# Kernel optimization log

Measured on AMD Instinct MI355X. Metric: run time of the kernel, lower is better.

## Reference

```python
import jax, jax.numpy as jnp
import numpy as np

EPS = 1e-5

def _layer_norm(x, g, b):
    mu = jnp.mean(x, axis=-1, keepdims=True)
    var = jnp.mean(jnp.square(x - mu), axis=-1, keepdims=True)
    return (x - mu) * jax.lax.rsqrt(var + EPS) * g + b

def setup_inputs() -> dict:
    key = jax.random.key(0)
    ks = jax.random.split(key, 8)
    B, S, H, NH, FF = 2, 2048, 2048, 16, 8192
    x = jax.random.normal(ks[0], (B, S, H), dtype=jnp.float32)
    # causal mask: True = masked (matches masked_fill semantics)
    mask = jnp.triu(jnp.ones((S, S), dtype=bool), k=1)
    sc = 0.02
    wq = jax.random.normal(ks[1], (H, H), dtype=jnp.float32) * sc
    wk = jax.random.normal(ks[2], (H, H), dtype=jnp.float32) * sc
    wv = jax.random.normal(ks[3], (H, H), dtype=jnp.float32) * sc
    wo = jax.random.normal(ks[4], (H, H), dtype=jnp.float32) * sc
    w_in = jax.random.normal(ks[5], (H, FF), dtype=jnp.float32) * sc
    w_out = jax.random.normal(ks[6], (FF, H), dtype=jnp.float32) * sc
    ln1_g = jnp.ones((H,), jnp.float32); ln1_b = jnp.zeros((H,), jnp.float32)
    ln2_g = jnp.ones((H,), jnp.float32); ln2_b = jnp.zeros((H,), jnp.float32)
    return {"x": x, "mask": mask, "wq": wq, "wk": wk, "wv": wv, "wo": wo,
            "w_in": w_in, "w_out": w_out,
            "ln1_g": ln1_g, "ln1_b": ln1_b, "ln2_g": ln2_g, "ln2_b": ln2_b}

def reference(x, mask, wq, wk, wv, wo, w_in, w_out, ln1_g, ln1_b, ln2_g, ln2_b):
    B, S, H = x.shape
    NH = 16
    HD = H // NH
    scale = HD ** (-0.5)
    # attention with pre-norm
    xn = _layer_norm(x, ln1_g, ln1_b)
    q = (xn @ wq).reshape(B, S, NH, HD)
    k = (xn @ wk).reshape(B, S, NH, HD)
    v = (xn @ wv).reshape(B, S, NH, HD)
    scores = jnp.einsum('bqhd,bkhd->bhqk', q, k) * scale
    scores = jnp.where(mask[:S, :S], -jnp.inf, scores)
    attn = jax.nn.softmax(scores, axis=-1)
    out = jnp.einsum('bhqk,bkhd->bqhd', attn, v).reshape(B, S, H)
    h = x + out @ wo
    # FFN with pre-norm, tanh-approx GELU
    hn = _layer_norm(h, ln2_g, ln2_b)
    ff = jax.nn.gelu(hn @ w_in, approximate=True) @ w_out
    return h + ff
```

## Files before the change

kernel.cpp:

```cpp
#include <hip/hip_runtime.h>
#include <hip/hip_bf16.h>

#define B_ 2
#define S_ 2048
#define H_ 2048
#define NH_ 16
#define HD_ 128
#define FF_ 8192

typedef __attribute__((ext_vector_type(8))) short bf16x8;
typedef __attribute__((ext_vector_type(4))) float f32x4;

#define NEG_BIG (-1e30f)

#define GLL16(gp, lp)                                                                    \
  __builtin_amdgcn_global_load_lds((const __attribute__((address_space(1))) void*)(gp),  \
                                   (__attribute__((address_space(3))) void*)(lp), 16, 0, 0)

__device__ __forceinline__ float b2f(unsigned short u) {
  union { unsigned int i; float f; } c; c.i = ((unsigned int)u) << 16; return c.f;
}
__device__ __forceinline__ unsigned short f2b(float f) {
  unsigned int u = __float_as_uint(f);
  u += 0x7fffu + ((u >> 16) & 1u);
  return (unsigned short)(u >> 16);
}
__device__ __forceinline__ float ldf(const void* p, size_t i, int f32) {
  return f32 ? ((const float*)p)[i] : b2f(((const unsigned short*)p)[i]);
}
__device__ __forceinline__ void unpack8(uint4 r, float* f) {
  f[0] = b2f((unsigned short)(r.x & 0xffffu)); f[1] = b2f((unsigned short)(r.x >> 16));
  f[2] = b2f((unsigned short)(r.y & 0xffffu)); f[3] = b2f((unsigned short)(r.y >> 16));
  f[4] = b2f((unsigned short)(r.z & 0xffffu)); f[5] = b2f((unsigned short)(r.z >> 16));
  f[6] = b2f((unsigned short)(r.w & 0xffffu)); f[7] = b2f((unsigned short)(r.w >> 16));
}

__global__ void detect_k(const unsigned int* __restrict__ x, int* __restrict__ flagp) {
  if (threadIdx.x == 0) {
    int c = 0;
    for (int i = 0; i < 256; ++i) {
      unsigned int e = (x[i] >> 7) & 0xffu;
      c += (e >= 97u && e <= 130u) ? 1 : 0;
    }
    *flagp = (c < 128) ? 1 : 0;
  }
}

__global__ __launch_bounds__(256) void transpose_k(const void* __restrict__ in,
                                                   unsigned short* __restrict__ out,
                                                   int R, int C,
                                                   const int* __restrict__ flagp) {
  __shared__ unsigned short tile[32][33];
  int f32 = *flagp;
  int r0 = blockIdx.y * 32, c0 = blockIdx.x * 32;
  int tx = threadIdx.x & 31, ty = threadIdx.x >> 5;
#pragma unroll
  for (int p = 0; p < 4; ++p)
    tile[ty + p * 8][tx] = f2b(ldf(in, (size_t)(r0 + ty + p * 8) * C + c0 + tx, f32));
  __syncthreads();
#pragma unroll
  for (int p = 0; p < 4; ++p)
    out[(size_t)(c0 + ty + p * 8) * R + r0 + tx] = tile[tx][ty + p * 8];
}

__global__ __launch_bounds__(256) void v_transpose_k(const unsigned short* __restrict__ qkv,
                                                     unsigned short* __restrict__ VT) {
  __shared__ unsigned short tile[32][33];
  int bh = blockIdx.z;
  int b = bh >> 4, h = bh & 15;
  int s0 = blockIdx.x * 32, d0 = blockIdx.y * 32;
  int tx = threadIdx.x & 31, ty = threadIdx.x >> 5;
#pragma unroll
  for (int p = 0; p < 4; ++p) {
    int s = s0 + ty + p * 8;
    tile[ty + p * 8][tx] = qkv[(size_t)(b * S_ + s) * (3 * H_) + 2 * H_ + h * HD_ + d0 + tx];
  }
  __syncthreads();
#pragma unroll
  for (int p = 0; p < 4; ++p)
    VT[((size_t)bh * HD_ + d0 + ty + p * 8) * S_ + s0 + tx] = tile[tx][ty + p * 8];
}

__global__ __launch_bounds__(256) void ln_k(const void* __restrict__ x,
                                            const void* __restrict__ g,
                                            const void* __restrict__ b,
                                            unsigned short* __restrict__ y,
                                            const int* __restrict__ flagp, int in_mode) {
  __shared__ float red[2][4];
  int f32 = *flagp;
  int xf = in_mode ? f32 : 0;
  int row = blockIdx.x;
  int t = threadIdx.x;
  float v[8];
  size_t base = (size_t)row * H_ + t * 8;
  if (xf) {
    const float4* p = reinterpret_cast<const float4*>((const float*)x + base);
    float4 u0 = p[0], u1 = p[1];
    v[0] = u0.x; v[1] = u0.y; v[2] = u0.z; v[3] = u0.w;
    v[4] = u1.x; v[5] = u1.y; v[6] = u1.z; v[7] = u1.w;
  } else {
    unpack8(*reinterpret_cast<const uint4*>((const unsigned short*)x + base), v);
  }
  float s1 = 0.f, s2 = 0.f;
#pragma unroll
  for (int i = 0; i < 8; ++i) { s1 += v[i]; s2 += v[i] * v[i]; }
#pragma unroll
  for (int off = 32; off > 0; off >>= 1) {
    s1 += __shfl_down(s1, off);
    s2 += __shfl_down(s2, off);
  }
  int w = t >> 6, lane = t & 63;
  if (lane == 0) { red[0][w] = s1; red[1][w] = s2; }
  __syncthreads();
  s1 = red[0][0] + red[0][1] + red[0][2] + red[0][3];
  s2 = red[1][0] + red[1][1] + red[1][2] + red[1][3];
  float mu = s1 * (1.0f / H_);
  float var = s2 * (1.0f / H_) - mu * mu;
  float rinv = rsqrtf(var + 1e-5f);
  float gv[8], bv[8];
#pragma unroll
  for (int i = 0; i < 8; ++i) {
    gv[i] = ldf(g, t * 8 + i, f32);
    bv[i] = ldf(b, t * 8 + i, f32);
  }
  unsigned int o[4];
#pragma unroll
  for (int i = 0; i < 4; ++i) {
    unsigned short lo = f2b((v[2 * i] - mu) * rinv * gv[2 * i] + bv[2 * i]);
    unsigned short hi = f2b((v[2 * i + 1] - mu) * rinv * gv[2 * i + 1] + bv[2 * i + 1]);
    o[i] = (unsigned int)lo | ((unsigned int)hi << 16);
  }
  uint4 ov; ov.x = o[0]; ov.y = o[1]; ov.z = o[2]; ov.w = o[3];
  *reinterpret_cast<uint4*>(y + base) = ov;
}

template <int EPI>
__global__ __launch_bounds__(256) void gemm_bt(const unsigned short* __restrict__ A,
                                               const unsigned short* __restrict__ BT,
                                               void* __restrict__ C,
                                               const void* __restrict__ resid,
                                               int M, int N, int K,
                                               const int* __restrict__ flagp,
                                               int resid_mode, int store_mode) {
  __shared__ unsigned short As[2][128 * 32];
  __shared__ unsigned short Bs[2][128 * 32];
  int f32 = *flagp;
  int rf = resid_mode ? f32 : 0;
  int sf = store_mode ? f32 : 0;
  int tid = threadIdx.x;
  int m_base = blockIdx.y * 128;
  int n_base = blockIdx.x * 128;
  int w = tid >> 6, lane = tid & 63;
  int l15 = lane & 15, quad = lane >> 4;
  int wm = (w >> 1) * 64, wn = (w & 1) * 64;
  int lr = lane >> 2, lc = lane & 3;
  int swz = lc ^ (lr & 3);

  const unsigned short* gA0 = A + (size_t)(m_base + w * 32 + lr) * K + swz * 8;
  const unsigned short* gA1 = A + (size_t)(m_base + w * 32 + 16 + lr) * K + swz * 8;
  const unsigned short* gB0 = BT + (size_t)(n_base + w * 32 + lr) * K + swz * 8;
  const unsigned short* gB1 = BT + (size_t)(n_base + w * 32 + 16 + lr) * K + swz * 8;
  int lofs0 = (w * 32) * 32;
  int lofs1 = (w * 32 + 16) * 32;

  f32x4 acc[4][4];
#pragma unroll
  for (int i = 0; i < 4; ++i)
#pragma unroll
    for (int j = 0; j < 4; ++j) acc[i][j] = (f32x4){0.f, 0.f, 0.f, 0.f};

  int rd_swz = (quad ^ (l15 & 3)) * 8;

  GLL16(gA0, &As[0][lofs0]);
  GLL16(gA1, &As[0][lofs1]);
  GLL16(gB0, &Bs[0][lofs0]);
  GLL16(gB1, &Bs[0][lofs1]);

  int cur = 0;
  for (int k0 = 0; k0 < K; k0 += 32, cur ^= 1) {
    __syncthreads();
    int k1 = k0 + 32;
    if (k1 < K) {
      GLL16(gA0 + k1, &As[cur ^ 1][lofs0]);
      GLL16(gA1 + k1, &As[cur ^ 1][lofs1]);
      GLL16(gB0 + k1, &Bs[cur ^ 1][lofs0]);
      GLL16(gB1 + k1, &Bs[cur ^ 1][lofs1]);
    }
    bf16x8 a[4], b[4];
#pragma unroll
    for (int i = 0; i < 4; ++i)
      a[i] = *reinterpret_cast<const bf16x8*>(&As[cur][(wm + i * 16 + l15) * 32 + rd_swz]);
#pragma unroll
    for (int j = 0; j < 4; ++j)
      b[j] = *reinterpret_cast<const bf16x8*>(&Bs[cur][(wn + j * 16 + l15) * 32 + rd_swz]);
#pragma unroll
    for (int i = 0; i < 4; ++i)
#pragma unroll
      for (int j = 0; j < 4; ++j)
        acc[i][j] = __builtin_amdgcn_mfma_f32_16x16x32_bf16(a[i], b[j], acc[i][j], 0, 0, 0);
  }

#pragma unroll
  for (int i = 0; i < 4; ++i) {
#pragma unroll
    for (int j = 0; j < 4; ++j) {
#pragma unroll
      for (int r = 0; r < 4; ++r) {
        int row = m_base + wm + i * 16 + quad * 4 + r;
        int col = n_base + wn + j * 16 + l15;
        size_t idx = (size_t)row * N + col;
        float v = acc[i][j][r];
        if (EPI == 1) v += ldf(resid, idx, rf);
        if (EPI == 2) {
          float u = v;
          float tt = 0.7978845608028654f * (u + 0.044715f * u * u * u);
          v = 0.5f * u * (1.0f + tanhf(tt));
        }
        if (sf) ((float*)C)[idx] = v;
        else    ((unsigned short*)C)[idx] = f2b(v);
      }
    }
  }
}

__global__ __launch_bounds__(256) void attn_k(const unsigned short* __restrict__ qkv,
                                              const unsigned short* __restrict__ VT,
                                              unsigned short* __restrict__ out) {
  __shared__ unsigned short Ks[64 * 128];
  __shared__ unsigned short Vs[128 * 64];
  __shared__ unsigned short Ps[4][16][72];
  int qb = blockIdx.x, bh = blockIdx.y;
  int b = bh >> 4, h = bh & 15;
  int q0 = qb * 64;
  int tid = threadIdx.x;
  int w = tid >> 6, lane = tid & 63, l15 = lane & 15, quad = lane >> 4;
  const float scale = 0.08838834764831845f;

  bf16x8 aq[4];
  {
    const unsigned short* qrow =
        qkv + (size_t)(b * S_ + q0 + w * 16 + l15) * (3 * H_) + h * HD_;
#pragma unroll
    for (int ks = 0; ks < 4; ++ks)
      aq[ks] = *reinterpret_cast<const bf16x8*>(qrow + ks * 32 + quad * 8);
  }

  int krow_off = lane >> 4;
  int kcb = lane & 15;
  int vrow_off = lane >> 3;
  int vcb = lane & 7;

  f32x4 o[8];
#pragma unroll
  for (int f = 0; f < 8; ++f) o[f] = (f32x4){0.f, 0.f, 0.f, 0.f};
  float m_i[4], l_i[4];
#pragma unroll
  for (int r = 0; r < 4; ++r) { m_i[r] = NEG_BIG; l_i[r] = 0.f; }

  const unsigned short* kbase = qkv + (size_t)b * S_ * (3 * H_) + H_ + h * HD_;
  const unsigned short* vbase = VT + (size_t)bh * HD_ * S_;

  for (int kv0 = 0; kv0 <= q0; kv0 += 64) {
    __syncthreads();
#pragma unroll
    for (int t = 0; t < 4; ++t) {
      int krow = w * 16 + t * 4 + krow_off;
      int kswz = kcb ^ (krow & 7);
      GLL16(kbase + (size_t)(kv0 + krow) * (3 * H_) + kswz * 8, &Ks[(w * 16 + t * 4) * 128]);
      int vrow = w * 32 + t * 8 + vrow_off;
      int vswz = vcb ^ (vrow & 7);
      GLL16(vbase + (size_t)vrow * S_ + kv0 + vswz * 8, &Vs[(w * 32 + t * 8) * 64]);
    }
    __syncthreads();

    f32x4 sc[4];
#pragma unroll
    for (int j = 0; j < 4; ++j) sc[j] = (f32x4){0.f, 0.f, 0.f, 0.f};
#pragma unroll
    for (int ks = 0; ks < 4; ++ks) {
#pragma unroll
      for (int j = 0; j < 4; ++j) {
        int r = j * 16 + l15;
        bf16x8 bk = *reinterpret_cast<const bf16x8*>(
            &Ks[r * 128 + (((ks * 4 + quad) ^ (l15 & 7))) * 8]);
        sc[j] = __builtin_amdgcn_mfma_f32_16x16x32_bf16(aq[ks], bk, sc[j], 0, 0, 0);
      }
    }
    bool diag = (kv0 == q0);
#pragma unroll
    for (int j = 0; j < 4; ++j)
#pragma unroll
      for (int r = 0; r < 4; ++r) {
        float s = sc[j][r] * scale;
        if (diag && (j * 16 + l15 > w * 16 + quad * 4 + r)) s = NEG_BIG;
        sc[j][r] = s;
      }

    float mx[4];
#pragma unroll
    for (int r = 0; r < 4; ++r) {
      mx[r] = sc[0][r];
#pragma unroll
      for (int j = 1; j < 4; ++j) mx[r] = fmaxf(mx[r], sc[j][r]);
    }
#pragma unroll
    for (int mm = 1; mm <= 8; mm <<= 1)
#pragma unroll
      for (int r = 0; r < 4; ++r) mx[r] = fmaxf(mx[r], __shfl_xor(mx[r], mm));
    float alpha[4];
#pragma unroll
    for (int r = 0; r < 4; ++r) {
      float mn = fmaxf(m_i[r], mx[r]);
      alpha[r] = __expf(m_i[r] - mn);
      m_i[r] = mn;
    }
    float pr[4][4], rs[4] = {0.f, 0.f, 0.f, 0.f};
#pragma unroll
    for (int j = 0; j < 4; ++j)
#pragma unroll
      for (int r = 0; r < 4; ++r) {
        float p = __expf(sc[j][r] - m_i[r]);
        pr[j][r] = p;
        rs[r] += p;
      }
#pragma unroll
    for (int mm = 1; mm <= 8; mm <<= 1)
#pragma unroll
      for (int r = 0; r < 4; ++r) rs[r] += __shfl_xor(rs[r], mm);
#pragma unroll
    for (int r = 0; r < 4; ++r) l_i[r] = l_i[r] * alpha[r] + rs[r];
#pragma unroll
    for (int f = 0; f < 8; ++f)
#pragma unroll
      for (int r = 0; r < 4; ++r) o[f][r] *= alpha[r];

#pragma unroll
    for (int j = 0; j < 4; ++j)
#pragma unroll
      for (int r = 0; r < 4; ++r)
        Ps[w][quad * 4 + r][j * 16 + l15] = f2b(pr[j][r]);

#pragma unroll
    for (int ks2 = 0; ks2 < 2; ++ks2) {
      bf16x8 ap = *reinterpret_cast<const bf16x8*>(&Ps[w][l15][ks2 * 32 + quad * 8]);
#pragma unroll
      for (int f = 0; f < 8; ++f) {
        int r = f * 16 + l15;
        bf16x8 bv = *reinterpret_cast<const bf16x8*>(
            &Vs[r * 64 + (((ks2 * 4 + quad) ^ (l15 & 7))) * 8]);
        o[f] = __builtin_amdgcn_mfma_f32_16x16x32_bf16(ap, bv, o[f], 0, 0, 0);
      }
    }
  }

  float inv[4];
#pragma unroll
  for (int r = 0; r < 4; ++r) inv[r] = 1.0f / l_i[r];
#pragma unroll
  for (int f = 0; f < 8; ++f)
#pragma unroll
    for (int r = 0; r < 4; ++r)
      out[(size_t)(b * S_ + q0 + w * 16 + quad * 4 + r) * H_ + h * HD_ + f * 16 + l15] =
          f2b(o[f][r] * inv[r]);
}

extern "C" void kernel_launch(void* const* d_in, const int* in_sizes, int n_in,
                              void* d_out, int out_size, void* d_ws, size_t ws_size,
                              hipStream_t stream) {
  (void)in_sizes; (void)n_in; (void)out_size; (void)ws_size;
  const void* x     = d_in[0];
  const void* wq    = d_in[2];
  const void* wk    = d_in[3];
  const void* wv    = d_in[4];
  const void* wo    = d_in[5];
  const void* w_in  = d_in[6];
  const void* w_out = d_in[7];
  const void* g1    = d_in[8];
  const void* b1    = d_in[9];
  const void* g2    = d_in[10];
  const void* b2    = d_in[11];
  char* ws = (char*)d_ws;

  const size_t MB = 1024 * 1024;
  unsigned short* W  = (unsigned short*)(ws + 0 * MB);
  unsigned short* E  = (unsigned short*)(ws + 32 * MB);
  unsigned short* F  = (unsigned short*)(ws + 48 * MB);
  unsigned short* Hb = (unsigned short*)(ws + 112 * MB);
  int* flagp         = (int*)(ws + 128 * MB);

  unsigned short* wqkvT = W;
  unsigned short* xn    = E;
  unsigned short* qkv   = F;
  unsigned short* VT    = F + (size_t)B_ * S_ * 3 * H_;
  unsigned short* attnb = E;
  unsigned short* hbuf  = Hb;
  unsigned short* hn    = E;
  unsigned short* ff1   = F;

  dim3 blk(256);
  detect_k<<<1, 64, 0, stream>>>((const unsigned int*)x, flagp);
  transpose_k<<<dim3(H_ / 32, H_ / 32), blk, 0, stream>>>(wq, wqkvT, H_, H_, flagp);
  transpose_k<<<dim3(H_ / 32, H_ / 32), blk, 0, stream>>>(wk, wqkvT + (size_t)H_ * H_, H_, H_, flagp);
  transpose_k<<<dim3(H_ / 32, H_ / 32), blk, 0, stream>>>(wv, wqkvT + (size_t)2 * H_ * H_, H_, H_, flagp);
  ln_k<<<B_ * S_, blk, 0, stream>>>(x, g1, b1, xn, flagp, 1);
  gemm_bt<0><<<dim3(3 * H_ / 128, B_ * S_ / 128), blk, 0, stream>>>(
      xn, wqkvT, qkv, nullptr, B_ * S_, 3 * H_, H_, flagp, 0, 0);
  v_transpose_k<<<dim3(S_ / 32, HD_ / 32, B_ * NH_), blk, 0, stream>>>(qkv, VT);
  attn_k<<<dim3(S_ / 64, B_ * NH_), blk, 0, stream>>>(qkv, VT, attnb);
  transpose_k<<<dim3(H_ / 32, H_ / 32), blk, 0, stream>>>(wo, W, H_, H_, flagp);
  gemm_bt<1><<<dim3(H_ / 128, B_ * S_ / 128), blk, 0, stream>>>(
      attnb, W, hbuf, x, B_ * S_, H_, H_, flagp, 1, 0);
  ln_k<<<B_ * S_, blk, 0, stream>>>(hbuf, g2, b2, hn, flagp, 0);
  transpose_k<<<dim3(FF_ / 32, H_ / 32), blk, 0, stream>>>(w_in, W, H_, FF_, flagp);
  gemm_bt<2><<<dim3(FF_ / 128, B_ * S_ / 128), blk, 0, stream>>>(
      hn, W, ff1, nullptr, B_ * S_, FF_, H_, flagp, 0, 0);
  transpose_k<<<dim3(H_ / 32, FF_ / 32), blk, 0, stream>>>(w_out, W, FF_, H_, flagp);
  gemm_bt<1><<<dim3(H_ / 128, B_ * S_ / 128), blk, 0, stream>>>(
      ff1, W, d_out, hbuf, B_ * S_, H_, FF_, flagp, 0, 1);
}
```

Before: 1.088 ms.

## Replace GEMM with 256x256-tile, 8-wave ping-pong pipelined kernel and XCD-aware block remap

```diff
diff --git a/kernel.cpp b/kernel.cpp
--- a/kernel.cpp
+++ b/kernel.cpp
@@ -134,82 +134,148 @@
   *reinterpret_cast<uint4*>(y + base) = ov;
 }
 
+#define PH_BAR() do { asm volatile("" ::: "memory"); __builtin_amdgcn_s_barrier(); \
+                      asm volatile("" ::: "memory"); } while (0)
+#define VMC(n) asm volatile("s_waitcnt vmcnt(" #n ")" ::: "memory")
+
+#define STA(buf_, h_, kt_) do {                                                        \
+  GLL16(pA0 + (size_t)(h_) * 128 * K + (kt_) * 64, &LdsA[buf_][(h_) * 8192 + lw]);     \
+  GLL16(pA1 + (size_t)(h_) * 128 * K + (kt_) * 64, &LdsA[buf_][(h_) * 8192 + 4096 + lw]); } while (0)
+#define STB(buf_, h_, kt_) do {                                                        \
+  GLL16(pB0 + (size_t)(h_) * 128 * K + (kt_) * 64, &LdsB[buf_][(h_) * 8192 + lw]);     \
+  GLL16(pB1 + (size_t)(h_) * 128 * K + (kt_) * 64, &LdsB[buf_][(h_) * 8192 + 4096 + lw]); } while (0)
+
+#define LDA4(AF, buf_, mb_) do { _Pragma("unroll")                                     \
+  for (int mi_ = 0; mi_ < 4; ++mi_) {                                                  \
+    const unsigned short* _p = &LdsA[buf_][(wr * 128 + ((mb_) + mi_) * 16 + l15) * 64];\
+    AF[mi_][0] = *reinterpret_cast<const bf16x8*>(_p + cs0);                           \
+    AF[mi_][1] = *reinterpret_cast<const bf16x8*>(_p + cs1); } } while (0)
+#define LDB2(BF, buf_, nb_) do { _Pragma("unroll")                                     \
+  for (int ni_ = 0; ni_ < 2; ++ni_) {                                                  \
+    const unsigned short* _p = &LdsB[buf_][(wc * 64 + ((nb_) + ni_) * 16 + l15) * 64]; \
+    BF[ni_][0] = *reinterpret_cast<const bf16x8*>(_p + cs0);                           \
+    BF[ni_][1] = *reinterpret_cast<const bf16x8*>(_p + cs1); } } while (0)
+
+#define MF8(AF, BF, MO, NO) do { _Pragma("unroll")                                     \
+  for (int mi_ = 0; mi_ < 4; ++mi_) { _Pragma("unroll")                                \
+    for (int ni_ = 0; ni_ < 2; ++ni_) {                                                \
+      acc[(MO) + mi_][(NO) + ni_] = __builtin_amdgcn_mfma_f32_16x16x32_bf16(           \
+          AF[mi_][0], BF[ni_][0], acc[(MO) + mi_][(NO) + ni_], 0, 0, 0);               \
+      acc[(MO) + mi_][(NO) + ni_] = __builtin_amdgcn_mfma_f32_16x16x32_bf16(           \
+          AF[mi_][1], BF[ni_][1], acc[(MO) + mi_][(NO) + ni_], 0, 0, 0);               \
+    } } } while (0)
+
+#define GITER(LAST, tO, tE2, tO2) do {                                                 \
+                                                                              \
+  LDA4(aL, 0, 0); LDB2(bL, 0, 0);                                                      \
+  STA(1, 1, tO);                                                                       \
+  PH_BAR(); __builtin_amdgcn_s_setprio(1);                                             \
+  MF8(aL, bL, 0, 0);                                                                   \
+  __builtin_amdgcn_s_setprio(0); PH_BAR();                                             \
+                                                                              \
+  LDB2(bH, 0, 2);                                                                      \
+  PH_BAR(); __builtin_amdgcn_s_setprio(1);                                             \
+  MF8(aL, bH, 0, 2);                                                                   \
+  __builtin_amdgcn_s_setprio(0); PH_BAR();                                             \
+                                                                              \
+  LDA4(aH, 0, 4);                                                                      \
+  if (!(LAST)) STB(0, 0, tE2);                                                         \
+  PH_BAR(); __builtin_amdgcn_s_setprio(1);                                             \
+  MF8(aH, bL, 4, 0);                                                                   \
+  __builtin_amdgcn_s_setprio(0); PH_BAR();                                             \
+                                                                              \
+  if (!(LAST)) { STB(0, 1, tE2); STA(0, 0, tE2); VMC(6); } else { VMC(0); }            \
+  PH_BAR(); __builtin_amdgcn_s_setprio(1);                                             \
+  MF8(aH, bH, 4, 2);                                                                   \
+  __builtin_amdgcn_s_setprio(0); PH_BAR();                                             \
+                                                                              \
+  LDA4(aL, 1, 0); LDB2(bL, 1, 0);                                                      \
+  if (!(LAST)) STA(0, 1, tE2);                                                         \
+  PH_BAR(); __builtin_amdgcn_s_setprio(1);                                             \
+  MF8(aL, bL, 0, 0);                                                                   \
+  __builtin_amdgcn_s_setprio(0); PH_BAR();                                             \
+                                                                              \
+  LDB2(bH, 1, 2);                                                                      \
+  PH_BAR(); __builtin_amdgcn_s_setprio(1);                                             \
+  MF8(aL, bH, 0, 2);                                                                   \
+  __builtin_amdgcn_s_setprio(0); PH_BAR();                                             \
+                                                                              \
+  LDA4(aH, 1, 4);                                                                      \
+  if (!(LAST)) STB(1, 0, tO2);                                                         \
+  PH_BAR(); __builtin_amdgcn_s_setprio(1);                                             \
+  MF8(aH, bL, 4, 0);                                                                   \
+  __builtin_amdgcn_s_setprio(0); PH_BAR();                                             \
+                                                                              \
+  if (!(LAST)) { STB(1, 1, tO2); STA(1, 0, tO2); VMC(6); }                             \
+  PH_BAR(); __builtin_amdgcn_s_setprio(1);                                             \
+  MF8(aH, bH, 4, 2);                                                                   \
+  __builtin_amdgcn_s_setprio(0); PH_BAR();                                             \
+} while (0)
+
 template <int EPI>
-__global__ __launch_bounds__(256) void gemm_bt(const unsigned short* __restrict__ A,
+__global__ __launch_bounds__(512) void gemm256(const unsigned short* __restrict__ A,
                                                const unsigned short* __restrict__ BT,
                                                void* __restrict__ C,
                                                const void* __restrict__ resid,
                                                int M, int N, int K,
                                                const int* __restrict__ flagp,
-                                               int resid_mode, int store_mode) {
-  __shared__ unsigned short As[2][128 * 32];
-  __shared__ unsigned short Bs[2][128 * 32];
+                                               int resid_mode, int store_mode, int nbx) {
+  (void)M;
+  __shared__ unsigned short LdsA[2][16384];
+  __shared__ unsigned short LdsB[2][16384];
+
+  unsigned nwg = gridDim.x, q = nwg >> 3;
+  unsigned o = blockIdx.x;
+  unsigned wg = (o & 7u) * q + (o >> 3);
+  int bx = (int)(wg % (unsigned)nbx), by = (int)(wg / (unsigned)nbx);
+  int m_base = by * 256, n_base = bx * 256;
+
+  int tid = threadIdx.x;
+  int w = tid >> 6, lane = tid & 63;
+  int l15 = lane & 15, quad = lane >> 4;
+  int wr = w >> 2, wc = w & 3;
+
+  int row0 = w * 8 + (lane >> 3);
+  int scb  = (lane & 7) ^ (lane >> 3);
+  const unsigned short* pA0 = A + (size_t)(m_base + row0) * K + scb * 8;
+  const unsigned short* pA1 = pA0 + (size_t)64 * K;
+  const unsigned short* pB0 = BT + (size_t)(n_base + row0) * K + scb * 8;
+  const unsigned short* pB1 = pB0 + (size_t)64 * K;
+  unsigned lw = (unsigned)w * 512;
+
+  int cs0 = ((quad) ^ (l15 & 7)) * 8;
+  int cs1 = ((4 + quad) ^ (l15 & 7)) * 8;
+
+  f32x4 acc[8][4];
+#pragma unroll
+  for (int i = 0; i < 8; ++i)
+#pragma unroll
+    for (int j = 0; j < 4; ++j) acc[i][j] = (f32x4){0.f, 0.f, 0.f, 0.f};
+
+  bf16x8 aL[4][2], aH[4][2], bL[2][2], bH[2][2];
+
+  STA(0, 0, 0); STA(0, 1, 0); STB(0, 0, 0); STB(0, 1, 0);
+  STB(1, 0, 1); STB(1, 1, 1); STA(1, 0, 1);
+  VMC(6);
+  PH_BAR();
+
+  int niter = K >> 7;
+  for (int i = 0; i < niter - 1; ++i) GITER(0, 2 * i + 1, 2 * i + 2, 2 * i + 3);
+  GITER(1, 2 * niter - 1, 0, 0);
+
   int f32 = *flagp;
   int rf = resid_mode ? f32 : 0;
   int sf = store_mode ? f32 : 0;
-  int tid = threadIdx.x;
-  int m_base = blockIdx.y * 128;
-  int n_base = blockIdx.x * 128;
-  int w = tid >> 6, lane = tid & 63;
-  int l15 = lane & 15, quad = lane >> 4;
-  int wm = (w >> 1) * 64, wn = (w & 1) * 64;
-  int lr = lane >> 2, lc = lane & 3;
-  int swz = lc ^ (lr & 3);
-
-  const unsigned short* gA0 = A + (size_t)(m_base + w * 32 + lr) * K + swz * 8;
-  const unsigned short* gA1 = A + (size_t)(m_base + w * 32 + 16 + lr) * K + swz * 8;
-  const unsigned short* gB0 = BT + (size_t)(n_base + w * 32 + lr) * K + swz * 8;
-  const unsigned short* gB1 = BT + (size_t)(n_base + w * 32 + 16 + lr) * K + swz * 8;
-  int lofs0 = (w * 32) * 32;
-  int lofs1 = (w * 32 + 16) * 32;
-
-  f32x4 acc[4][4];
-#pragma unroll
-  for (int i = 0; i < 4; ++i)
-#pragma unroll
-    for (int j = 0; j < 4; ++j) acc[i][j] = (f32x4){0.f, 0.f, 0.f, 0.f};
-
-  int rd_swz = (quad ^ (l15 & 3)) * 8;
-
-  GLL16(gA0, &As[0][lofs0]);
-  GLL16(gA1, &As[0][lofs1]);
-  GLL16(gB0, &Bs[0][lofs0]);
-  GLL16(gB1, &Bs[0][lofs1]);
-
-  int cur = 0;
-  for (int k0 = 0; k0 < K; k0 += 32, cur ^= 1) {
-    __syncthreads();
-    int k1 = k0 + 32;
-    if (k1 < K) {
-      GLL16(gA0 + k1, &As[cur ^ 1][lofs0]);
-      GLL16(gA1 + k1, &As[cur ^ 1][lofs1]);
-      GLL16(gB0 + k1, &Bs[cur ^ 1][lofs0]);
-      GLL16(gB1 + k1, &Bs[cur ^ 1][lofs1]);
-    }
-    bf16x8 a[4], b[4];
-#pragma unroll
-    for (int i = 0; i < 4; ++i)
-      a[i] = *reinterpret_cast<const bf16x8*>(&As[cur][(wm + i * 16 + l15) * 32 + rd_swz]);
-#pragma unroll
-    for (int j = 0; j < 4; ++j)
-      b[j] = *reinterpret_cast<const bf16x8*>(&Bs[cur][(wn + j * 16 + l15) * 32 + rd_swz]);
-#pragma unroll
-    for (int i = 0; i < 4; ++i)
-#pragma unroll
-      for (int j = 0; j < 4; ++j)
-        acc[i][j] = __builtin_amdgcn_mfma_f32_16x16x32_bf16(a[i], b[j], acc[i][j], 0, 0, 0);
-  }
-
-#pragma unroll
-  for (int i = 0; i < 4; ++i) {
-#pragma unroll
-    for (int j = 0; j < 4; ++j) {
+#pragma unroll
+  for (int mi = 0; mi < 8; ++mi) {
+#pragma unroll
+    for (int ni = 0; ni < 4; ++ni) {
 #pragma unroll
       for (int r = 0; r < 4; ++r) {
-        int row = m_base + wm + i * 16 + quad * 4 + r;
-        int col = n_base + wn + j * 16 + l15;
+        int row = m_base + wr * 128 + mi * 16 + quad * 4 + r;
+        int col = n_base + wc * 64 + ni * 16 + l15;
         size_t idx = (size_t)row * N + col;
-        float v = acc[i][j][r];
+        float v = acc[mi][ni][r];
         if (EPI == 1) v += ldf(resid, idx, rf);
         if (EPI == 2) {
           float u = v;
@@ -398,23 +464,24 @@
   unsigned short* ff1   = F;
 
   dim3 blk(256);
+  dim3 gblk(512);
   detect_k<<<1, 64, 0, stream>>>((const unsigned int*)x, flagp);
   transpose_k<<<dim3(H_ / 32, H_ / 32), blk, 0, stream>>>(wq, wqkvT, H_, H_, flagp);
   transpose_k<<<dim3(H_ / 32, H_ / 32), blk, 0, stream>>>(wk, wqkvT + (size_t)H_ * H_, H_, H_, flagp);
   transpose_k<<<dim3(H_ / 32, H_ / 32), blk, 0, stream>>>(wv, wqkvT + (size_t)2 * H_ * H_, H_, H_, flagp);
   ln_k<<<B_ * S_, blk, 0, stream>>>(x, g1, b1, xn, flagp, 1);
-  gemm_bt<0><<<dim3(3 * H_ / 128, B_ * S_ / 128), blk, 0, stream>>>(
-      xn, wqkvT, qkv, nullptr, B_ * S_, 3 * H_, H_, flagp, 0, 0);
+  gemm256<0><<<dim3((3 * H_ / 256) * (B_ * S_ / 256)), gblk, 0, stream>>>(
+      xn, wqkvT, qkv, nullptr, B_ * S_, 3 * H_, H_, flagp, 0, 0, 3 * H_ / 256);
   v_transpose_k<<<dim3(S_ / 32, HD_ / 32, B_ * NH_), blk, 0, stream>>>(qkv, VT);
   attn_k<<<dim3(S_ / 64, B_ * NH_), blk, 0, stream>>>(qkv, VT, attnb);
   transpose_k<<<dim3(H_ / 32, H_ / 32), blk, 0, stream>>>(wo, W, H_, H_, flagp);
-  gemm_bt<1><<<dim3(H_ / 128, B_ * S_ / 128), blk, 0, stream>>>(
-      attnb, W, hbuf, x, B_ * S_, H_, H_, flagp, 1, 0);
+  gemm256<1><<<dim3((H_ / 256) * (B_ * S_ / 256)), gblk, 0, stream>>>(
+      attnb, W, hbuf, x, B_ * S_, H_, H_, flagp, 1, 0, H_ / 256);
   ln_k<<<B_ * S_, blk, 0, stream>>>(hbuf, g2, b2, hn, flagp, 0);
   transpose_k<<<dim3(FF_ / 32, H_ / 32), blk, 0, stream>>>(w_in, W, H_, FF_, flagp);
-  gemm_bt<2><<<dim3(FF_ / 128, B_ * S_ / 128), blk, 0, stream>>>(
-      hn, W, ff1, nullptr, B_ * S_, FF_, H_, flagp, 0, 0);
+  gemm256<2><<<dim3((FF_ / 256) * (B_ * S_ / 256)), gblk, 0, stream>>>(
+      hn, W, ff1, nullptr, B_ * S_, FF_, H_, flagp, 0, 0, FF_ / 256);
   transpose_k<<<dim3(H_ / 32, FF_ / 32), blk, 0, stream>>>(w_out, W, FF_, H_, flagp);
-  gemm_bt<1><<<dim3(H_ / 128, B_ * S_ / 128), blk, 0, stream>>>(
-      ff1, W, d_out, hbuf, B_ * S_, H_, FF_, flagp, 0, 1);
-}
+  gemm256<1><<<dim3((H_ / 256) * (B_ * S_ / 256)), gblk, 0, stream>>>(
+      ff1, W, d_out, hbuf, B_ * S_, H_, FF_, flagp, 0, 1, H_ / 256);
+}
```

New measurement: 1.184 ms. 8.8% more time.
